# Optimization experiments

Measured on AMD Instinct MI355X. Metric: run time of the kernel, lower is better.

Reference implementation:

```python
import jax, jax.numpy as jnp
import numpy as np

SIZE = 384  # output resolution
SCALE = (0.8, 1.0)


def _bilinear_crop_resize(img, cs, top, left):
    """img: [C,H,W]; cs/top/left: int32 scalars. Crop [top:top+cs, left:left+cs],
    resize to SIZE x SIZE with bilinear, align_corners=False (PyTorch semantics)."""
    csf = cs.astype(jnp.float32)
    # source coords within the crop, clamped like PyTorch (src = max(src,0), upper bounded)
    coords = (jnp.arange(SIZE, dtype=jnp.float32) + 0.5) * (csf / SIZE) - 0.5
    coords = jnp.clip(coords, 0.0, csf - 1.0)
    i0 = jnp.floor(coords).astype(jnp.int32)
    i1 = jnp.minimum(i0 + 1, cs - 1)
    w = coords - i0.astype(jnp.float32)  # [SIZE]
    y0, y1 = i0 + top, i1 + top
    x0, x1 = i0 + left, i1 + left
    wy, wx = w[:, None], w[None, :]
    g = lambda yy, xx: img[:, yy[:, None], xx[None, :]]  # [C,SIZE,SIZE]
    return (g(y0, x0) * (1 - wy) * (1 - wx)
            + g(y0, x1) * (1 - wy) * wx
            + g(y1, x0) * wy * (1 - wx)
            + g(y1, x1) * wy * wx)


def _nearest_crop_resize(msk, cs, top, left):
    """msk: [1,H,W]. PyTorch mode='nearest': src_idx = floor(dst * in/out)."""
    idx = jnp.floor(jnp.arange(SIZE, dtype=jnp.float32) * cs.astype(jnp.float32) / SIZE).astype(jnp.int32)
    idx = jnp.minimum(idx, cs - 1)
    y, x = idx + top, idx + left
    return msk[:, y[:, None], x[None, :]]


def setup_inputs() -> dict:
    key = jax.random.key(0)
    k1, k2, k3, k4, k5 = jax.random.split(key, 5)
    B, C, H, W = 32, 3, 512, 512
    image = jax.random.normal(k1, (B, C, H, W), dtype=jnp.float32)
    mask = (jax.random.uniform(k2, (B, 1, H, W)) > 0.5).astype(jnp.float32)
    scale = jax.random.uniform(k3, (B,), minval=SCALE[0], maxval=SCALE[1])
    crop_size = (scale * min(H, W)).astype(jnp.int32)
    max_y = (H - crop_size).astype(jnp.float32)
    max_x = (W - crop_size).astype(jnp.float32)
    top = jnp.where(max_y > 0, jnp.floor(jax.random.uniform(k4, (B,)) * max_y), 0.0).astype(jnp.int32)
    left = jnp.where(max_x > 0, jnp.floor(jax.random.uniform(k5, (B,)) * max_x), 0.0).astype(jnp.int32)
    return {"image": image, "mask": mask, "crop_size": crop_size, "top": top, "left": left}


def reference(image, mask, crop_size, top, left):
    img_out = jax.vmap(_bilinear_crop_resize)(image, crop_size, top, left)
    msk_out = jax.vmap(_nearest_crop_resize)(mask, crop_size, top, left)
    return img_out, msk_out
```

## Files before the change

### kernel.cpp

```cpp
#include <hip/hip_runtime.h>


constexpr int OUT = 384;
constexpr int H = 512;
constexpr int W = 512;
constexpr int B = 32;
constexpr int C = 3;
constexpr int BLOCKS_PER_B = (OUT * OUT) / 256;
constexpr int NBLK = B * BLOCKS_PER_B;
constexpr int BLOCKS_PER_XCD = NBLK / 8;

__global__ __launch_bounds__(256) void rrc_pair_kernel(
    const float* __restrict__ image,
    const float* __restrict__ mask,
    const int* __restrict__ crop_size,
    const int* __restrict__ top,
    const int* __restrict__ left,
    float* __restrict__ img_out,
    float* __restrict__ msk_out)
{
    const int hw = blockIdx.x;
    const int logical = (hw & 7) * BLOCKS_PER_XCD + (hw >> 3);

    const int b   = logical / BLOCKS_PER_B;
    const int pix = (logical % BLOCKS_PER_B) * 256 + (int)threadIdx.x;
    const int j = pix % OUT;
    const int i = pix / OUT;

    const int cs = crop_size[b];
    const int t  = top[b];
    const int l  = left[b];
    const float csf = (float)cs;
    const float s   = csf / (float)OUT;

    float cy = ((float)i + 0.5f) * s - 0.5f;
    cy = fminf(fmaxf(cy, 0.0f), csf - 1.0f);
    int   iy0 = (int)floorf(cy);
    int   iy1 = min(iy0 + 1, cs - 1);
    float wy  = cy - (float)iy0;

    float cx = ((float)j + 0.5f) * s - 0.5f;
    cx = fminf(fmaxf(cx, 0.0f), csf - 1.0f);
    int   ix0 = (int)floorf(cx);
    int   ix1 = min(ix0 + 1, cs - 1);
    float wx  = cx - (float)ix0;

    const int y0 = iy0 + t, y1 = iy1 + t;
    const int x0 = ix0 + l, x1 = ix1 + l;

    const float w00 = (1.0f - wy) * (1.0f - wx);
    const float w01 = (1.0f - wy) * wx;
    const float w10 = wy * (1.0f - wx);
    const float w11 = wy * wx;

    const float* imgb = image + (size_t)b * C * H * W;
    const size_t o_base = (size_t)b * C * OUT * OUT + (size_t)i * OUT + (size_t)j;

    #pragma unroll
    for (int c = 0; c < C; ++c) {
        const float* p = imgb + (size_t)c * H * W;
        float v00 = p[(size_t)y0 * W + x0];
        float v01 = p[(size_t)y0 * W + x1];
        float v10 = p[(size_t)y1 * W + x0];
        float v11 = p[(size_t)y1 * W + x1];
        float r = v00 * w00 + v01 * w01 + v10 * w10 + v11 * w11;
        __builtin_nontemporal_store(r, img_out + o_base + (size_t)c * OUT * OUT);
    }

    int my = (i * cs) / OUT; my = min(my, cs - 1);
    int mx = (j * cs) / OUT; mx = min(mx, cs - 1);
    float mval = mask[((size_t)b * H + (size_t)(my + t)) * W + (mx + l)];
    __builtin_nontemporal_store(mval, msk_out + ((size_t)b * OUT + i) * OUT + j);
}

extern "C" void kernel_launch(void* const* d_in, const int* in_sizes, int n_in,
                              void* d_out, int out_size, void* d_ws, size_t ws_size,
                              hipStream_t stream) {
    const float* image = (const float*)d_in[0];
    const float* mask  = (const float*)d_in[1];
    const int* cs      = (const int*)d_in[2];
    const int* top     = (const int*)d_in[3];
    const int* left    = (const int*)d_in[4];

    float* img_out = (float*)d_out;
    float* msk_out = img_out + (size_t)B * C * OUT * OUT;

    dim3 block(256);
    dim3 grid(NBLK);
    hipLaunchKernelGGL(rrc_pair_kernel, grid, block, 0, stream,
                       image, mask, cs, top, left, img_out, msk_out);
}
```

Before: 36.42 us.

## Stage source rows in LDS with one block per output row

The grid is remapped so each 384-thread block produces one full output row, with one thread per output column. The block first loads, with vectorized loads, the two full 512-wide source rows for all three channels into shared memory, syncs once, then does the bilinear gathers from LDS instead of global memory. The mask load is issued before the barrier so its latency overlaps the staging. This trades scattered global gathers for coalesced row loads plus a barrier, and it reads whole rows even when the crop is narrower.

```diff
diff --git a/kernel.cpp b/kernel.cpp
--- a/kernel.cpp
+++ b/kernel.cpp
@@ -6,11 +6,12 @@
 constexpr int W = 512;
 constexpr int B = 32;
 constexpr int C = 3;
-constexpr int BLOCKS_PER_B = (OUT * OUT) / 256;
-constexpr int NBLK = B * BLOCKS_PER_B;
-constexpr int BLOCKS_PER_XCD = NBLK / 8;
+constexpr int NBLK = B * OUT;
+constexpr int BPX  = NBLK / 8;
 
-__global__ __launch_bounds__(256) void rrc_pair_kernel(
+typedef float f32x4 __attribute__((ext_vector_type(4)));
+
+__global__ __launch_bounds__(384) void rrc_pair_kernel(
     const float* __restrict__ image,
     const float* __restrict__ mask,
     const int* __restrict__ crop_size,
@@ -19,13 +20,13 @@
     float* __restrict__ img_out,
     float* __restrict__ msk_out)
 {
+    __shared__ float lds[2 * C][W];
+
     const int hw = blockIdx.x;
-    const int logical = (hw & 7) * BLOCKS_PER_XCD + (hw >> 3);
-
-    const int b   = logical / BLOCKS_PER_B;
-    const int pix = (logical % BLOCKS_PER_B) * 256 + (int)threadIdx.x;
-    const int j = pix % OUT;
-    const int i = pix / OUT;
+    const int logical = (hw & 7) * BPX + (hw >> 3);
+    const int b = logical / OUT;
+    const int i = logical % OUT;
+    const int tid = (int)threadIdx.x;
 
     const int cs = crop_size[b];
     const int t  = top[b];
@@ -38,14 +39,35 @@
     int   iy0 = (int)floorf(cy);
     int   iy1 = min(iy0 + 1, cs - 1);
     float wy  = cy - (float)iy0;
+    const int y0 = iy0 + t, y1 = iy1 + t;
 
+    const float* imgb = image + (size_t)b * C * H * W;
+
+    {
+        const int base = tid * 8;
+        const int r    = base >> 9;
+        const int col  = base & 511;
+        const int c    = r >> 1;
+        const int y    = (r & 1) ? y1 : y0;
+        const float* src = imgb + ((size_t)c * H + (size_t)y) * W + col;
+        f32x4 a0 = *(const f32x4*)src;
+        f32x4 a1 = *(const f32x4*)(src + 4);
+        *(f32x4*)&lds[r][col]     = a0;
+        *(f32x4*)&lds[r][col + 4] = a1;
+    }
+
+    int my = (i * cs) / OUT;   my = min(my, cs - 1);
+    int mx = (tid * cs) / OUT; mx = min(mx, cs - 1);
+    const float mval = mask[((size_t)b * H + (size_t)(my + t)) * W + (mx + l)];
+
+    __syncthreads();
+
+    const int j = tid;
     float cx = ((float)j + 0.5f) * s - 0.5f;
     cx = fminf(fmaxf(cx, 0.0f), csf - 1.0f);
     int   ix0 = (int)floorf(cx);
     int   ix1 = min(ix0 + 1, cs - 1);
     float wx  = cx - (float)ix0;
-
-    const int y0 = iy0 + t, y1 = iy1 + t;
     const int x0 = ix0 + l, x1 = ix1 + l;
 
     const float w00 = (1.0f - wy) * (1.0f - wx);
@@ -53,24 +75,20 @@
     const float w10 = wy * (1.0f - wx);
     const float w11 = wy * wx;
 
-    const float* imgb = image + (size_t)b * C * H * W;
     const size_t o_base = (size_t)b * C * OUT * OUT + (size_t)i * OUT + (size_t)j;
 
     #pragma unroll
     for (int c = 0; c < C; ++c) {
-        const float* p = imgb + (size_t)c * H * W;
-        float v00 = p[(size_t)y0 * W + x0];
-        float v01 = p[(size_t)y0 * W + x1];
-        float v10 = p[(size_t)y1 * W + x0];
-        float v11 = p[(size_t)y1 * W + x1];
+        float v00 = lds[c * 2][x0];
+        float v01 = lds[c * 2][x1];
+        float v10 = lds[c * 2 + 1][x0];
+        float v11 = lds[c * 2 + 1][x1];
         float r = v00 * w00 + v01 * w01 + v10 * w10 + v11 * w11;
         __builtin_nontemporal_store(r, img_out + o_base + (size_t)c * OUT * OUT);
     }
 
-    int my = (i * cs) / OUT; my = min(my, cs - 1);
-    int mx = (j * cs) / OUT; mx = min(mx, cs - 1);
-    float mval = mask[((size_t)b * H + (size_t)(my + t)) * W + (mx + l)];
-    __builtin_nontemporal_store(mval, msk_out + ((size_t)b * OUT + i) * OUT + j);
+    __builtin_nontemporal_store(mval,
+        msk_out + (size_t)b * OUT * OUT + (size_t)i * OUT + (size_t)j);
 }
 
 extern "C" void kernel_launch(void* const* d_in, const int* in_sizes, int n_in,
@@ -85,7 +103,7 @@
     float* img_out = (float*)d_out;
     float* msk_out = img_out + (size_t)B * C * OUT * OUT;
 
-    dim3 block(256);
+    dim3 block(384);
     dim3 grid(NBLK);
     hipLaunchKernelGGL(rrc_pair_kernel, grid, block, 0, stream,
                        image, mask, cs, top, left, img_out, msk_out);
```

Result: faster. 33.09 us (-9.1%).
